# Performance work log

Hardware: AMD Instinct MI355X
Metric: run time of the kernel (lower is better)

Reference implementation:

```python
import jax, jax.numpy as jnp
import numpy as np

N_ = 512   # batch / num users
M_ = 254   # num UAV nodes -> size S = M_ + 2 = 256
D_ = 2     # coordinate dim
H_ = 128   # pointer-net hidden dim


def setup_inputs() -> dict:
    key = jax.random.key(0)
    ks = jax.random.split(key, 7)
    s = 0.1
    return {
        "outputs": jax.random.normal(ks[0], (2 * N_ + M_, D_), dtype=jnp.float32),
        "W_embed": jax.random.normal(ks[1], (D_, H_), dtype=jnp.float32) * s,
        "b_embed": jnp.zeros((H_,), jnp.float32),
        "lstm_Wi": jax.random.normal(ks[2], (H_, 4 * H_), dtype=jnp.float32) * s,
        "lstm_Wh": jax.random.normal(ks[3], (H_, 4 * H_), dtype=jnp.float32) * s,
        "lstm_b": jnp.zeros((4 * H_,), jnp.float32),
        "att_W1": jax.random.normal(ks[4], (H_, H_), dtype=jnp.float32) * s,
        "att_W2": jax.random.normal(ks[5], (H_, H_), dtype=jnp.float32) * s,
        "att_v": jax.random.normal(ks[6], (H_,), dtype=jnp.float32) * s,
        "N": N_,
    }


def _rgnn_loss(outputs, W_embed, b_embed, lstm_Wi, lstm_Wh, lstm_b,
               att_W1, att_W2, att_v, N):
    D = outputs.shape[1]
    H = W_embed.shape[1]
    M = outputs.shape[0] - 2 * N
    users_src = outputs[:N][:, None, :]                         # (B,1,D)
    users_dst = outputs[N:2 * N][:, None, :]                    # (B,1,D)
    uav_nodes = jnp.broadcast_to(outputs[2 * N:][None, :, :], (N, M, D))
    uav_graph = jnp.concatenate([users_src, uav_nodes, users_dst], axis=1)  # (B,S,D)
    B, S = uav_graph.shape[0], uav_graph.shape[1]
    NEG = jnp.float32(-np.inf)

    # pointer-net: node embeddings and step-independent attention projection
    e_all = uav_graph @ W_embed + b_embed                       # (B,S,H)
    W1e = jnp.einsum('bsh,hk->bsk', e_all, att_W1)              # (B,S,H)
    rows = jnp.arange(B)

    mask0 = jnp.zeros((B, S), jnp.float32).at[:, 0].set(NEG)
    x0 = uav_graph[:, 0, :]                                     # start at src
    carry0 = (x0, x0,
              jnp.zeros((B, H), jnp.float32), jnp.zeros((B, H), jnp.float32),
              mask0, jnp.zeros((B,), jnp.float32))

    def step(carry, k):
        x, Y0, h, c, mask, max_dist = carry
        # dst node blocked only at step 0, re-opened afterwards
        mask = mask.at[:, -1].set(jnp.where(k == 0, NEG, 0.0))
        # LSTM cell on embedded current node
        e_x = x @ W_embed + b_embed                             # (B,H)
        gates = e_x @ lstm_Wi + h @ lstm_Wh + lstm_b            # (B,4H)
        i, f, g, o = jnp.split(gates, 4, axis=1)
        c = jax.nn.sigmoid(f) * c + jax.nn.sigmoid(i) * jnp.tanh(g)
        h = jax.nn.sigmoid(o) * jnp.tanh(c)
        # additive attention pointer logits
        q = h @ att_W2                                          # (B,H)
        logits = jnp.tanh(W1e + q[:, None, :]) @ att_v + mask   # (B,S)
        logits = jax.lax.stop_gradient(logits)                  # output.detach()
        idx = jnp.argmax(logits, axis=1)                        # (B,)
        Y1 = uav_graph[rows, idx]                               # (B,D)
        dist = jnp.sqrt(jnp.sum((Y1 - Y0) ** 2, axis=1) + 1e-12)
        max_dist = jnp.maximum(max_dist, dist)
        mask = mask.at[rows, idx].add(NEG)
        mask = jnp.where((idx == S)[:, None], NEG, mask)
        return (Y1, Y1, h, c, mask, max_dist), None

    (_, _, _, _, _, max_dist), _ = jax.lax.scan(step, carry0, jnp.arange(S))
    return max_dist.mean()


def reference(outputs, W_embed, b_embed, lstm_Wi, lstm_Wh, lstm_b,
              att_W1, att_W2, att_v, N):
    return _rgnn_loss(outputs, W_embed, b_embed, lstm_Wi, lstm_Wh, lstm_b,
                      att_W1, att_W2, att_v, N)
```

## Files before the change

### kernel.cpp

```cpp
#include <hip/hip_runtime.h>
#include <math.h>

#define NB   512
#define MM   254
#define SS   256
#define HH   128
#define RTOT 1278
#define NBLK 256

#define C2   2.885390081777927f
#define C1   1.442695040888963f

__device__ __forceinline__ float rcpf(float x)  { return __builtin_amdgcn_rcpf(x); }
__device__ __forceinline__ float exp2f_(float x){ return __builtin_amdgcn_exp2f(x); }
__device__ __forceinline__ float sigm2(float x)  { return rcpf(1.0f + exp2f_(-C1 * x)); }
__device__ __forceinline__ float tanh2(float x)  { return 1.0f - 2.0f * rcpf(1.0f + exp2f_(C2 * x)); }

__global__ __launch_bounds__(128) void precompute_k(
    const float* __restrict__ outputs, const float* __restrict__ Wemb,
    const float* __restrict__ bemb, const float* __restrict__ Wi,
    const float* __restrict__ W1, const float* __restrict__ lb,
    float4* __restrict__ EWiP, float4* __restrict__ W1eQ)
{
  int r = blockIdx.x;
  int t = threadIdx.x;
  __shared__ float e[HH];
  __shared__ float w1e[HH];
  float px = outputs[2 * r], py = outputs[2 * r + 1];
  e[t] = px * Wemb[t] + py * Wemb[HH + t] + bemb[t];
  __syncthreads();
  float acc = 0.f;
#pragma unroll 8
  for (int h = 0; h < HH; ++h) acc = fmaf(e[h], W1[h * HH + t], acc);
  w1e[t] = acc;
  float g4[4];
#pragma unroll
  for (int c = 0; c < 4; ++c) {
    int j = t + c * HH;
    float a = 0.f;
#pragma unroll 8
    for (int h = 0; h < HH; ++h) a = fmaf(e[h], Wi[h * 512 + j], a);
    g4[c] = a + lb[j];
  }
  float4 v4; v4.x = g4[0]; v4.y = g4[1]; v4.z = g4[2]; v4.w = g4[3];
  EWiP[(size_t)r * HH + t] = v4;
  __syncthreads();
  if (t < 32) {
    float4 p;
    p.x = C2 * w1e[4 * t];     p.y = C2 * w1e[4 * t + 1];
    p.z = C2 * w1e[4 * t + 2]; p.w = C2 * w1e[4 * t + 3];
    W1eQ[(size_t)t * RTOT + r] = p;
  }
}

__global__ __launch_bounds__(128) void transpose_k(
    const float* __restrict__ Wh, const float* __restrict__ W2,
    float* __restrict__ WhT, float* __restrict__ W2T)
{
  int bidx = blockIdx.x;
  int k = threadIdx.x;
  if (bidx < 512) WhT[(size_t)bidx * 128 + k] = Wh[(size_t)k * 512 + bidx];
  else {
    int j = bidx - 512;
    W2T[(size_t)j * 128 + k] = W2[(size_t)k * 128 + j];
  }
}

__global__ __launch_bounds__(1024) void decode_k(
    const float* __restrict__ outputs, const float* __restrict__ WhT,
    const float* __restrict__ Wh, const float* __restrict__ W2T,
    const float* __restrict__ av,
    const float4* __restrict__ EWiP, const float4* __restrict__ W1eQ,
    float* __restrict__ maxd_out)
{
  const int t = threadIdx.x;
  const int bid = blockIdx.x;

  __shared__ float WhL[64][512];
  __shared__ float posU[2 * MM];
  __shared__ float dstS[2][2];
  __shared__ __align__(16) float hS[2][HH];
  __shared__ __align__(16) float qS[2][HH];
  __shared__ __align__(16) float vS2[HH];
  __shared__ float sumvS[2];
  __shared__ float pS[2][2][512];
  __shared__ float lp[2][2][SS];
  __shared__ int   lsS[2][SS];
  __shared__ int   actS[2][254];
  __shared__ int   cntS[2], curS[2];

  const int gj  = t >> 1;
  const int gh  = t & 1;
  const int cg  = t >> 9;
  const int cj  = (t >> 2) & 127;
  const int ckq = t & 3;
  const int lg  = t >> 9;
  const int lhf = (t >> 8) & 1;
  const int lu  = t & 255;

  for (int i = t; i < 64 * 512; i += 1024) ((float*)WhL)[i] = Wh[64 * 512 + i];
  for (int i = t; i < 2 * MM; i += 1024)   posU[i] = outputs[4 * NB + i];
  if (t < 256) { int g = t >> 7, j = t & 127; hS[g][j] = 0.f; }
  if (t < HH) vS2[t] = -2.0f * av[t];
  if (t >= 256 && t < 258) {
    int half = t - 256; float s = 0.f;
    for (int h = half * 64; h < half * 64 + 64; ++h) s += av[h];
    sumvS[half] = s;
  }
  if (t < 254) actS[0][t] = t + 1;
  else if (t >= 512 && t < 766) actS[1][t - 512] = t - 511;
  if (t == 0) {
    cntS[0] = 254; curS[0] = bid;
    dstS[0][0] = outputs[2 * (NB + bid)]; dstS[0][1] = outputs[2 * (NB + bid) + 1];
  }
  if (t == 512) {
    cntS[1] = 254; curS[1] = bid + NBLK;
    dstS[1][0] = outputs[2 * (NB + bid + NBLK)];
    dstS[1][1] = outputs[2 * (NB + bid + NBLK) + 1];
  }
  __syncthreads();

  float px = 0.f, py = 0.f, md = 0.f;
  if (t == 0)   { px = outputs[2 * bid];          py = outputs[2 * bid + 1]; }
  if (t == 512) { px = outputs[2 * (bid + NBLK)]; py = outputs[2 * (bid + NBLK) + 1]; }

  float creg = 0.f;

  for (int k = 0; k < SS; ++k) {
    float4 ew4 = make_float4(0.f, 0.f, 0.f, 0.f);
    if (t < 256) ew4 = EWiP[(size_t)curS[t >> 7] * HH + (t & 127)];
    {
      const float4* wg4 = (const float4*)(WhT + (size_t)gj * 128 + gh * 32);
      float4 wb[8];
#pragma unroll
      for (int i = 0; i < 8; ++i) wb[i] = wg4[i];
      float a0G = 0.f, a1G = 0.f, a0L = 0.f, a1L = 0.f;
      {
        const float* wl = &WhL[gh * 32][gj];
        const float4* hb0 = (const float4*)(&hS[0][64 + gh * 32]);
        const float4* hb1 = (const float4*)(&hS[1][64 + gh * 32]);
#pragma unroll
        for (int i = 0; i < 8; ++i) {
          float4 h0 = hb0[i], h1 = hb1[i];
          float wa = wl[(size_t)(4 * i) * 512];
          float wbv = wl[(size_t)(4 * i + 1) * 512];
          float wc = wl[(size_t)(4 * i + 2) * 512];
          float wd = wl[(size_t)(4 * i + 3) * 512];
          a0L = fmaf(h0.x, wa, a0L); a0L = fmaf(h0.y, wbv, a0L);
          a0L = fmaf(h0.z, wc, a0L); a0L = fmaf(h0.w, wd, a0L);
          a1L = fmaf(h1.x, wa, a1L); a1L = fmaf(h1.y, wbv, a1L);
          a1L = fmaf(h1.z, wc, a1L); a1L = fmaf(h1.w, wd, a1L);
        }
      }
      {
        const float4* hb0 = (const float4*)(&hS[0][gh * 32]);
        const float4* hb1 = (const float4*)(&hS[1][gh * 32]);
#pragma unroll
        for (int i = 0; i < 8; ++i) {
          float4 h0 = hb0[i], h1 = hb1[i];
          float4 w = wb[i];
          a0G = fmaf(h0.x, w.x, a0G); a0G = fmaf(h0.y, w.y, a0G);
          a0G = fmaf(h0.z, w.z, a0G); a0G = fmaf(h0.w, w.w, a0G);
          a1G = fmaf(h1.x, w.x, a1G); a1G = fmaf(h1.y, w.y, a1G);
          a1G = fmaf(h1.z, w.z, a1G); a1G = fmaf(h1.w, w.w, a1G);
        }
      }
      pS[0][gh][gj] = a0G + a0L;
      pS[1][gh][gj] = a1G + a1L;
    }
    __syncthreads();

    if (t < 256) {
      int g = t >> 7, jj = t & 127;
      float ei = ew4.x + (pS[g][0][jj]       + pS[g][1][jj]);
      float ef = ew4.y + (pS[g][0][128 + jj] + pS[g][1][128 + jj]);
      float eg = ew4.z + (pS[g][0][256 + jj] + pS[g][1][256 + jj]);
      float eo = ew4.w + (pS[g][0][384 + jj] + pS[g][1][384 + jj]);
      float iv = sigm2(ei), fv = sigm2(ef), gv = tanh2(eg), ov = sigm2(eo);
      float cn = fv * creg + iv * gv;
      creg = cn;
      hS[g][jj] = ov * tanh2(cn);
    }
    __syncthreads();

    {
      const float4* w4 = (const float4*)(W2T + (size_t)cj * 128 + ckq * 32);
      const float4* h4 = (const float4*)(&hS[cg][ckq * 32]);
      float p0 = 0.f, p1 = 0.f;
#pragma unroll
      for (int i = 0; i < 8; ++i) {
        float4 w = w4[i], h = h4[i];
        p0 = fmaf(h.x, w.x, p0); p1 = fmaf(h.y, w.y, p1);
        p0 = fmaf(h.z, w.z, p0); p1 = fmaf(h.w, w.w, p1);
      }
      float p = p0 + p1;
      p += __shfl_xor(p, 1);
      p += __shfl_xor(p, 2);
      if (ckq == 0) qS[cg][cj] = C2 * p;
    }
    __syncthreads();

    {
      int cnt = cntS[lg];
      int cntEff = cnt + (k > 0 ? 1 : 0);
      if (lu < cntEff) {
        int s = (lu == cnt) ? 255 : actS[lg][lu];
        int r = (s == 255) ? (NB + bid + (lg << 8)) : (2 * NB + s - 1);
        const float4* wp = W1eQ + (size_t)(lhf * 16) * RTOT + r;
        const float4* qv4 = (const float4*)(&qS[lg][lhf * 64]);
        const float4* vv4 = (const float4*)(&vS2[lhf * 64]);
        float c0 = 0.f, c1 = 0.f;
#pragma unroll 4
        for (int i = 0; i < 16; ++i) {
          float4 w = wp[(size_t)i * RTOT];
          float4 q = qv4[i];
          float4 v = vv4[i];
          c0 = fmaf(v.x, rcpf(1.0f + exp2f_(w.x + q.x)), c0);
          c1 = fmaf(v.y, rcpf(1.0f + exp2f_(w.y + q.y)), c1);
          c0 = fmaf(v.z, rcpf(1.0f + exp2f_(w.z + q.z)), c0);
          c1 = fmaf(v.w, rcpf(1.0f + exp2f_(w.w + q.w)), c1);
        }
        lp[lg][lhf][lu] = (c0 + c1) + sumvS[lhf];
        if (lhf == 0) lsS[lg][lu] = s;
      }
    }
    __syncthreads();

    if ((t < 64) || (t >= 512 && t < 576)) {
      int g = t >> 9;
      int lane = t & 63;
      int cnt = cntS[g];
      int cntEff = cnt + (k > 0 ? 1 : 0);
      float val = -INFINITY;
      unsigned key = 0xFFFFFFFFu;
#pragma unroll
      for (int c = 0; c < 4; ++c) {
        int u = lane + 64 * c;
        if (u < cntEff) {
          float v2 = lp[g][0][u] + lp[g][1][u];
          unsigned k2 = ((unsigned)lsS[g][u] << 16) | (unsigned)u;
          if (v2 > val || (v2 == val && k2 < key)) { val = v2; key = k2; }
        }
      }
#pragma unroll
      for (int off = 1; off < 64; off <<= 1) {
        float v2 = __shfl_xor(val, off);
        unsigned k2 = __shfl_xor(key, off);
        if (v2 > val || (v2 == val && k2 < key)) { val = v2; key = k2; }
      }
      if (lane == 0) {
        int s   = (int)(key >> 16);
        int pos = (int)(key & 0xFFFFu);
        int rn  = (s == 255) ? (NB + bid + (g << 8)) : (2 * NB + s - 1);
        float nx, ny;
        if (s == 255) { nx = dstS[g][0]; ny = dstS[g][1]; }
        else          { nx = posU[2 * (s - 1)]; ny = posU[2 * (s - 1) + 1]; }
        float dx = nx - px, dy = ny - py;
        float d = sqrtf(dx * dx + dy * dy + 1e-12f);
        if (d > md) md = d;
        px = nx; py = ny;
        curS[g] = rn;
        if (s != 255) { actS[g][pos] = actS[g][cnt - 1]; cntS[g] = cnt - 1; }
      }
    }
    __syncthreads();
  }

  if (t == 0)   maxd_out[bid] = md;
  if (t == 512) maxd_out[bid + NBLK] = md;
}

__global__ __launch_bounds__(512) void reduce_k(const float* __restrict__ maxd,
                                               float* __restrict__ out)
{
  __shared__ float s[512];
  int t = threadIdx.x;
  s[t] = maxd[t];
  __syncthreads();
  for (int off = 256; off > 0; off >>= 1) {
    if (t < off) s[t] += s[t + off];
    __syncthreads();
  }
  if (t == 0) out[0] = s[0] * (1.0f / 512.0f);
}

extern "C" void kernel_launch(void* const* d_in, const int* in_sizes, int n_in,
                              void* d_out, int out_size, void* d_ws, size_t ws_size,
                              hipStream_t stream) {
  const float* outputs = (const float*)d_in[0];
  const float* Wemb    = (const float*)d_in[1];
  const float* bemb    = (const float*)d_in[2];
  const float* Wi      = (const float*)d_in[3];
  const float* Wh      = (const float*)d_in[4];
  const float* lb      = (const float*)d_in[5];
  const float* W1      = (const float*)d_in[6];
  const float* W2      = (const float*)d_in[7];
  const float* av      = (const float*)d_in[8];

  float* ws    = (float*)d_ws;
  float4* EWiP = (float4*)ws;
  float4* W1eQ = (float4*)(ws + (size_t)RTOT * 512);
  float*  WhT  = ws + (size_t)RTOT * 512 + (size_t)RTOT * 128;
  float*  W2T  = WhT + (size_t)512 * 128;
  float*  maxd = W2T + (size_t)128 * 128;

  hipLaunchKernelGGL(transpose_k, dim3(640), dim3(128), 0, stream, Wh, W2, WhT, W2T);
  hipLaunchKernelGGL(precompute_k, dim3(RTOT), dim3(HH), 0, stream,
                     outputs, Wemb, bemb, Wi, W1, lb, EWiP, W1eQ);
  hipLaunchKernelGGL(decode_k, dim3(NBLK), dim3(1024), 0, stream,
                     outputs, WhT, Wh, W2T, av, EWiP, W1eQ, maxd);
  hipLaunchKernelGGL(reduce_k, dim3(1), dim3(512), 0, stream, maxd, (float*)d_out);
}
```

Baseline: 2.296 ms.

## Pipeline two batch teams in a skewed phase schedule and remap Wh matvec layout

```diff
diff --git a/kernel.cpp b/kernel.cpp
--- a/kernel.cpp
+++ b/kernel.cpp
@@ -13,8 +13,14 @@
 
 __device__ __forceinline__ float rcpf(float x)  { return __builtin_amdgcn_rcpf(x); }
 __device__ __forceinline__ float exp2f_(float x){ return __builtin_amdgcn_exp2f(x); }
-__device__ __forceinline__ float sigm2(float x)  { return rcpf(1.0f + exp2f_(-C1 * x)); }
-__device__ __forceinline__ float tanh2(float x)  { return 1.0f - 2.0f * rcpf(1.0f + exp2f_(C2 * x)); }
+__device__ __forceinline__ float sigm2(float x) { return rcpf(1.0f + exp2f_(-C1 * x)); }
+__device__ __forceinline__ float tanh2(float x) { return 1.0f - 2.0f * rcpf(1.0f + exp2f_(C2 * x)); }
+
+__device__ __forceinline__ float4 fma4(float s, float4 w, float4 a) {
+  a.x = fmaf(s, w.x, a.x); a.y = fmaf(s, w.y, a.y);
+  a.z = fmaf(s, w.z, a.z); a.w = fmaf(s, w.w, a.w);
+  return a;
+}
 
 __global__ __launch_bounds__(128) void precompute_k(
     const float* __restrict__ outputs, const float* __restrict__ Wemb,
@@ -54,27 +60,23 @@
 }
 
 __global__ __launch_bounds__(128) void transpose_k(
-    const float* __restrict__ Wh, const float* __restrict__ W2,
-    float* __restrict__ WhT, float* __restrict__ W2T)
+    const float* __restrict__ W2, float* __restrict__ W2T)
 {
-  int bidx = blockIdx.x;
-  int k = threadIdx.x;
-  if (bidx < 512) WhT[(size_t)bidx * 128 + k] = Wh[(size_t)k * 512 + bidx];
-  else {
-    int j = bidx - 512;
-    W2T[(size_t)j * 128 + k] = W2[(size_t)k * 128 + j];
-  }
+  int j = blockIdx.x, k = threadIdx.x;
+  W2T[(size_t)j * 128 + k] = W2[(size_t)k * 128 + j];
 }
 
 __global__ __launch_bounds__(1024) void decode_k(
-    const float* __restrict__ outputs, const float* __restrict__ WhT,
-    const float* __restrict__ Wh, const float* __restrict__ W2T,
-    const float* __restrict__ av,
+    const float* __restrict__ outputs, const float* __restrict__ Wh,
+    const float* __restrict__ W2T, const float* __restrict__ av,
     const float4* __restrict__ EWiP, const float4* __restrict__ W1eQ,
     float* __restrict__ maxd_out)
 {
   const int t = threadIdx.x;
   const int bid = blockIdx.x;
+  const int team  = t >> 9;
+  const int local = t & 511;
+  const int g = team;
 
   __shared__ float WhL[64][512];
   __shared__ float posU[2 * MM];
@@ -83,24 +85,15 @@
   __shared__ __align__(16) float qS[2][HH];
   __shared__ __align__(16) float vS2[HH];
   __shared__ float sumvS[2];
-  __shared__ float pS[2][2][512];
+  __shared__ __align__(16) float pS[2][4][512];
   __shared__ float lp[2][2][SS];
   __shared__ int   lsS[2][SS];
   __shared__ int   actS[2][254];
   __shared__ int   cntS[2], curS[2];
 
-  const int gj  = t >> 1;
-  const int gh  = t & 1;
-  const int cg  = t >> 9;
-  const int cj  = (t >> 2) & 127;
-  const int ckq = t & 3;
-  const int lg  = t >> 9;
-  const int lhf = (t >> 8) & 1;
-  const int lu  = t & 255;
-
   for (int i = t; i < 64 * 512; i += 1024) ((float*)WhL)[i] = Wh[64 * 512 + i];
   for (int i = t; i < 2 * MM; i += 1024)   posU[i] = outputs[4 * NB + i];
-  if (t < 256) { int g = t >> 7, j = t & 127; hS[g][j] = 0.f; }
+  if (t < 256) { int gg = t >> 7, j = t & 127; hS[gg][j] = 0.f; }
   if (t < HH) vS2[t] = -2.0f * av[t];
   if (t >= 256 && t < 258) {
     int half = t - 256; float s = 0.f;
@@ -121,153 +114,159 @@
   __syncthreads();
 
   float px = 0.f, py = 0.f, md = 0.f;
-  if (t == 0)   { px = outputs[2 * bid];          py = outputs[2 * bid + 1]; }
-  if (t == 512) { px = outputs[2 * (bid + NBLK)]; py = outputs[2 * (bid + NBLK) + 1]; }
+  if (local == 0) {
+    int b = bid + (g << 8);
+    px = outputs[2 * b]; py = outputs[2 * b + 1];
+  }
 
   float creg = 0.f;
-
-  for (int k = 0; k < SS; ++k) {
-    float4 ew4 = make_float4(0.f, 0.f, 0.f, 0.f);
-    if (t < 256) ew4 = EWiP[(size_t)curS[t >> 7] * HH + (t & 127)];
-    {
-      const float4* wg4 = (const float4*)(WhT + (size_t)gj * 128 + gh * 32);
-      float4 wb[8];
-#pragma unroll
-      for (int i = 0; i < 8; ++i) wb[i] = wg4[i];
-      float a0G = 0.f, a1G = 0.f, a0L = 0.f, a1L = 0.f;
-      {
-        const float* wl = &WhL[gh * 32][gj];
-        const float4* hb0 = (const float4*)(&hS[0][64 + gh * 32]);
-        const float4* hb1 = (const float4*)(&hS[1][64 + gh * 32]);
+  float4 ew4 = make_float4(0.f, 0.f, 0.f, 0.f);
+
+  int ph = (team == 0) ? 0 : -2;
+  int lk = 0;
+
+  const int jq  = local & 127;
+  const int kq  = local >> 7;
+  const int cj  = (local >> 2) & 127;
+  const int ckq = local & 3;
+  const int lhf = local >> 8;
+  const int lu  = local & 255;
+
+  const int NSTAGE = 5 * SS + 2;
+  for (int sg = 0; sg < NSTAGE; ++sg) {
+    bool valid = (ph >= 0) && (lk < SS);
+    if (valid) {
+      if (ph == 0) {
+        if (local < 128) ew4 = EWiP[(size_t)curS[g] * HH + local];
+        float4 acc = make_float4(0.f, 0.f, 0.f, 0.f);
+        if (kq < 2) {
+          const float4* wg = (const float4*)(Wh + (size_t)(kq * 32) * 512) + jq;
+          const float4* h4 = (const float4*)(&hS[g][kq * 32]);
+          float4 wb[8];
+#pragma unroll
+          for (int b = 0; b < 4; ++b) {
+#pragma unroll
+            for (int i = 0; i < 8; ++i) wb[i] = wg[(size_t)(b * 8 + i) * 128];
+#pragma unroll
+            for (int i2 = 0; i2 < 2; ++i2) {
+              float4 h = h4[b * 2 + i2];
+              acc = fma4(h.x, wb[i2 * 4 + 0], acc);
+              acc = fma4(h.y, wb[i2 * 4 + 1], acc);
+              acc = fma4(h.z, wb[i2 * 4 + 2], acc);
+              acc = fma4(h.w, wb[i2 * 4 + 3], acc);
+            }
+          }
+        } else {
+          const float4* wl = (const float4*)(&WhL[(kq - 2) * 32][0]) + jq;
+          const float4* h4 = (const float4*)(&hS[g][kq * 32]);
+#pragma unroll
+          for (int i = 0; i < 8; ++i) {
+            float4 h  = h4[i];
+            float4 w0 = wl[(size_t)(4 * i + 0) * 128];
+            float4 w1 = wl[(size_t)(4 * i + 1) * 128];
+            float4 w2 = wl[(size_t)(4 * i + 2) * 128];
+            float4 w3 = wl[(size_t)(4 * i + 3) * 128];
+            acc = fma4(h.x, w0, acc);
+            acc = fma4(h.y, w1, acc);
+            acc = fma4(h.z, w2, acc);
+            acc = fma4(h.w, w3, acc);
+          }
+        }
+        *(float4*)&pS[g][kq][4 * jq] = acc;
+      } else if (ph == 1) {
+        if (local < 128) {
+          int jj = local;
+          float ei = ew4.x + ((pS[g][0][jj]       + pS[g][1][jj])       + (pS[g][2][jj]       + pS[g][3][jj]));
+          float ef = ew4.y + ((pS[g][0][128 + jj] + pS[g][1][128 + jj]) + (pS[g][2][128 + jj] + pS[g][3][128 + jj]));
+          float eg = ew4.z + ((pS[g][0][256 + jj] + pS[g][1][256 + jj]) + (pS[g][2][256 + jj] + pS[g][3][256 + jj]));
+          float eo = ew4.w + ((pS[g][0][384 + jj] + pS[g][1][384 + jj]) + (pS[g][2][384 + jj] + pS[g][3][384 + jj]));
+          float iv = sigm2(ei), fv = sigm2(ef), gv = tanh2(eg), ov = sigm2(eo);
+          float cn = fv * creg + iv * gv;
+          creg = cn;
+          hS[g][jj] = ov * tanh2(cn);
+        }
+      } else if (ph == 2) {
+        const float4* w4 = (const float4*)(W2T + (size_t)cj * 128 + ckq * 32);
+        const float4* h4 = (const float4*)(&hS[g][ckq * 32]);
+        float p0 = 0.f, p1 = 0.f;
 #pragma unroll
         for (int i = 0; i < 8; ++i) {
-          float4 h0 = hb0[i], h1 = hb1[i];
-          float wa = wl[(size_t)(4 * i) * 512];
-          float wbv = wl[(size_t)(4 * i + 1) * 512];
-          float wc = wl[(size_t)(4 * i + 2) * 512];
-          float wd = wl[(size_t)(4 * i + 3) * 512];
-          a0L = fmaf(h0.x, wa, a0L); a0L = fmaf(h0.y, wbv, a0L);
-          a0L = fmaf(h0.z, wc, a0L); a0L = fmaf(h0.w, wd, a0L);
-          a1L = fmaf(h1.x, wa, a1L); a1L = fmaf(h1.y, wbv, a1L);
-          a1L = fmaf(h1.z, wc, a1L); a1L = fmaf(h1.w, wd, a1L);
-        }
-      }
-      {
-        const float4* hb0 = (const float4*)(&hS[0][gh * 32]);
-        const float4* hb1 = (const float4*)(&hS[1][gh * 32]);
-#pragma unroll
-        for (int i = 0; i < 8; ++i) {
-          float4 h0 = hb0[i], h1 = hb1[i];
-          float4 w = wb[i];
-          a0G = fmaf(h0.x, w.x, a0G); a0G = fmaf(h0.y, w.y, a0G);
-          a0G = fmaf(h0.z, w.z, a0G); a0G = fmaf(h0.w, w.w, a0G);
-          a1G = fmaf(h1.x, w.x, a1G); a1G = fmaf(h1.y, w.y, a1G);
-          a1G = fmaf(h1.z, w.z, a1G); a1G = fmaf(h1.w, w.w, a1G);
-        }
-      }
-      pS[0][gh][gj] = a0G + a0L;
-      pS[1][gh][gj] = a1G + a1L;
-    }
-    __syncthreads();
-
-    if (t < 256) {
-      int g = t >> 7, jj = t & 127;
-      float ei = ew4.x + (pS[g][0][jj]       + pS[g][1][jj]);
-      float ef = ew4.y + (pS[g][0][128 + jj] + pS[g][1][128 + jj]);
-      float eg = ew4.z + (pS[g][0][256 + jj] + pS[g][1][256 + jj]);
-      float eo = ew4.w + (pS[g][0][384 + jj] + pS[g][1][384 + jj]);
-      float iv = sigm2(ei), fv = sigm2(ef), gv = tanh2(eg), ov = sigm2(eo);
-      float cn = fv * creg + iv * gv;
-      creg = cn;
-      hS[g][jj] = ov * tanh2(cn);
-    }
-    __syncthreads();
-
-    {
-      const float4* w4 = (const float4*)(W2T + (size_t)cj * 128 + ckq * 32);
-      const float4* h4 = (const float4*)(&hS[cg][ckq * 32]);
-      float p0 = 0.f, p1 = 0.f;
-#pragma unroll
-      for (int i = 0; i < 8; ++i) {
-        float4 w = w4[i], h = h4[i];
-        p0 = fmaf(h.x, w.x, p0); p1 = fmaf(h.y, w.y, p1);
-        p0 = fmaf(h.z, w.z, p0); p1 = fmaf(h.w, w.w, p1);
-      }
-      float p = p0 + p1;
-      p += __shfl_xor(p, 1);
-      p += __shfl_xor(p, 2);
-      if (ckq == 0) qS[cg][cj] = C2 * p;
-    }
-    __syncthreads();
-
-    {
-      int cnt = cntS[lg];
-      int cntEff = cnt + (k > 0 ? 1 : 0);
-      if (lu < cntEff) {
-        int s = (lu == cnt) ? 255 : actS[lg][lu];
-        int r = (s == 255) ? (NB + bid + (lg << 8)) : (2 * NB + s - 1);
-        const float4* wp = W1eQ + (size_t)(lhf * 16) * RTOT + r;
-        const float4* qv4 = (const float4*)(&qS[lg][lhf * 64]);
-        const float4* vv4 = (const float4*)(&vS2[lhf * 64]);
-        float c0 = 0.f, c1 = 0.f;
+          float4 w = w4[i], h = h4[i];
+          p0 = fmaf(h.x, w.x, p0); p1 = fmaf(h.y, w.y, p1);
+          p0 = fmaf(h.z, w.z, p0); p1 = fmaf(h.w, w.w, p1);
+        }
+        float p = p0 + p1;
+        p += __shfl_xor(p, 1);
+        p += __shfl_xor(p, 2);
+        if (ckq == 0) qS[g][cj] = C2 * p;
+      } else if (ph == 3) {
+        int cnt = cntS[g];
+        int cntEff = cnt + (lk > 0 ? 1 : 0);
+        if (lu < cntEff) {
+          int s = (lu == cnt) ? 255 : actS[g][lu];
+          int r = (s == 255) ? (NB + bid + (g << 8)) : (2 * NB + s - 1);
+          const float4* wp = W1eQ + (size_t)(lhf * 16) * RTOT + r;
+          const float4* qv4 = (const float4*)(&qS[g][lhf * 64]);
+          const float4* vv4 = (const float4*)(&vS2[lhf * 64]);
+          float c0 = 0.f, c1 = 0.f;
 #pragma unroll 4
-        for (int i = 0; i < 16; ++i) {
-          float4 w = wp[(size_t)i * RTOT];
-          float4 q = qv4[i];
-          float4 v = vv4[i];
-          c0 = fmaf(v.x, rcpf(1.0f + exp2f_(w.x + q.x)), c0);
-          c1 = fmaf(v.y, rcpf(1.0f + exp2f_(w.y + q.y)), c1);
-          c0 = fmaf(v.z, rcpf(1.0f + exp2f_(w.z + q.z)), c0);
-          c1 = fmaf(v.w, rcpf(1.0f + exp2f_(w.w + q.w)), c1);
-        }
-        lp[lg][lhf][lu] = (c0 + c1) + sumvS[lhf];
-        if (lhf == 0) lsS[lg][lu] = s;
+          for (int i = 0; i < 16; ++i) {
+            float4 w = wp[(size_t)i * RTOT];
+            float4 q = qv4[i];
+            float4 v = vv4[i];
+            c0 = fmaf(v.x, rcpf(1.0f + exp2f_(w.x + q.x)), c0);
+            c1 = fmaf(v.y, rcpf(1.0f + exp2f_(w.y + q.y)), c1);
+            c0 = fmaf(v.z, rcpf(1.0f + exp2f_(w.z + q.z)), c0);
+            c1 = fmaf(v.w, rcpf(1.0f + exp2f_(w.w + q.w)), c1);
+          }
+          lp[g][lhf][lu] = (c0 + c1) + sumvS[lhf];
+          if (lhf == 0) lsS[g][lu] = s;
+        }
+      } else {
+        if (local < 64) {
+          int lane = local;
+          int cnt = cntS[g];
+          int cntEff = cnt + (lk > 0 ? 1 : 0);
+          float val = -INFINITY;
+          unsigned key = 0xFFFFFFFFu;
+#pragma unroll
+          for (int c = 0; c < 4; ++c) {
+            int u = lane + 64 * c;
+            if (u < cntEff) {
+              float v2 = lp[g][0][u] + lp[g][1][u];
+              unsigned k2 = ((unsigned)lsS[g][u] << 16) | (unsigned)u;
+              if (v2 > val || (v2 == val && k2 < key)) { val = v2; key = k2; }
+            }
+          }
+#pragma unroll
+          for (int off = 1; off < 64; off <<= 1) {
+            float v2 = __shfl_xor(val, off);
+            unsigned k2 = __shfl_xor(key, off);
+            if (v2 > val || (v2 == val && k2 < key)) { val = v2; key = k2; }
+          }
+          if (lane == 0) {
+            int s   = (int)(key >> 16);
+            int pos = (int)(key & 0xFFFFu);
+            int rn  = (s == 255) ? (NB + bid + (g << 8)) : (2 * NB + s - 1);
+            float nx, ny;
+            if (s == 255) { nx = dstS[g][0]; ny = dstS[g][1]; }
+            else          { nx = posU[2 * (s - 1)]; ny = posU[2 * (s - 1) + 1]; }
+            float dx = nx - px, dy = ny - py;
+            float d = sqrtf(dx * dx + dy * dy + 1e-12f);
+            if (d > md) md = d;
+            px = nx; py = ny;
+            curS[g] = rn;
+            if (s != 255) { actS[g][pos] = actS[g][cnt - 1]; cntS[g] = cnt - 1; }
+          }
+        }
       }
     }
+    ++ph;
+    if (ph == 5) { ph = 0; ++lk; }
     __syncthreads();
-
-    if ((t < 64) || (t >= 512 && t < 576)) {
-      int g = t >> 9;
-      int lane = t & 63;
-      int cnt = cntS[g];
-      int cntEff = cnt + (k > 0 ? 1 : 0);
-      float val = -INFINITY;
-      unsigned key = 0xFFFFFFFFu;
-#pragma unroll
-      for (int c = 0; c < 4; ++c) {
-        int u = lane + 64 * c;
-        if (u < cntEff) {
-          float v2 = lp[g][0][u] + lp[g][1][u];
-          unsigned k2 = ((unsigned)lsS[g][u] << 16) | (unsigned)u;
-          if (v2 > val || (v2 == val && k2 < key)) { val = v2; key = k2; }
-        }
-      }
-#pragma unroll
-      for (int off = 1; off < 64; off <<= 1) {
-        float v2 = __shfl_xor(val, off);
-        unsigned k2 = __shfl_xor(key, off);
-        if (v2 > val || (v2 == val && k2 < key)) { val = v2; key = k2; }
-      }
-      if (lane == 0) {
-        int s   = (int)(key >> 16);
-        int pos = (int)(key & 0xFFFFu);
-        int rn  = (s == 255) ? (NB + bid + (g << 8)) : (2 * NB + s - 1);
-        float nx, ny;
-        if (s == 255) { nx = dstS[g][0]; ny = dstS[g][1]; }
-        else          { nx = posU[2 * (s - 1)]; ny = posU[2 * (s - 1) + 1]; }
-        float dx = nx - px, dy = ny - py;
-        float d = sqrtf(dx * dx + dy * dy + 1e-12f);
-        if (d > md) md = d;
-        px = nx; py = ny;
-        curS[g] = rn;
-        if (s != 255) { actS[g][pos] = actS[g][cnt - 1]; cntS[g] = cnt - 1; }
-      }
-    }
-    __syncthreads();
-  }
-
-  if (t == 0)   maxd_out[bid] = md;
-  if (t == 512) maxd_out[bid + NBLK] = md;
+  }
+
+  if (local == 0) maxd_out[bid + (g << 8)] = md;
 }
 
 __global__ __launch_bounds__(512) void reduce_k(const float* __restrict__ maxd,
@@ -300,14 +299,13 @@
   float* ws    = (float*)d_ws;
   float4* EWiP = (float4*)ws;
   float4* W1eQ = (float4*)(ws + (size_t)RTOT * 512);
-  float*  WhT  = ws + (size_t)RTOT * 512 + (size_t)RTOT * 128;
-  float*  W2T  = WhT + (size_t)512 * 128;
+  float*  W2T  = ws + (size_t)RTOT * 512 + (size_t)RTOT * 128;
   float*  maxd = W2T + (size_t)128 * 128;
 
-  hipLaunchKernelGGL(transpose_k, dim3(640), dim3(128), 0, stream, Wh, W2, WhT, W2T);
+  hipLaunchKernelGGL(transpose_k, dim3(128), dim3(128), 0, stream, W2, W2T);
   hipLaunchKernelGGL(precompute_k, dim3(RTOT), dim3(HH), 0, stream,
                      outputs, Wemb, bemb, Wi, W1, lb, EWiP, W1eQ);
   hipLaunchKernelGGL(decode_k, dim3(NBLK), dim3(1024), 0, stream,
-                     outputs, WhT, Wh, W2T, av, EWiP, W1eQ, maxd);
+                     outputs, Wh, W2T, av, EWiP, W1eQ, maxd);
   hipLaunchKernelGGL(reduce_k, dim3(1), dim3(512), 0, stream, maxd, (float*)d_out);
 }
```

Result: slower. 4.987 ms (+117.2%).
